# Optimization experiments

Hardware: AMD Instinct MI355X
Metric: run time of the kernel (lower is better)

Reference implementation:

```python
import jax, jax.numpy as jnp
import numpy as np

D_MODEL = 2048
N_HEADS = 32
N_KV_HEADS = 8
D_K = D_MODEL // N_HEADS
HEADS_PER_GROUP = N_HEADS // N_KV_HEADS
B, S = 2, 2048


def setup_inputs() -> dict:
    key = jax.random.key(0)
    ks = jax.random.split(key, 12)
    scale = 1.0 / np.sqrt(D_MODEL)
    inp = {
        "q": jax.random.normal(ks[0], (B, S, D_MODEL), jnp.float32),
        "k": jax.random.normal(ks[1], (B, S, D_MODEL), jnp.float32),
        "v": jax.random.normal(ks[2], (B, S, D_MODEL), jnp.float32),
        # causal mask, broadcastable over [B, H, S, S]
        "mask": jnp.tril(jnp.ones((S, S), jnp.bool_))[None, None],
        # torch Linear convention: W [out, in], y = x @ W.T + b
        "Wq": jax.random.normal(ks[3], (D_MODEL, D_MODEL), jnp.float32) * scale,
        "bq": jax.random.normal(ks[4], (D_MODEL,), jnp.float32) * 0.01,
        "Wk": jax.random.normal(ks[5], (N_KV_HEADS * D_K, D_MODEL), jnp.float32) * scale,
        "bk": jax.random.normal(ks[6], (N_KV_HEADS * D_K,), jnp.float32) * 0.01,
        "Wv": jax.random.normal(ks[7], (N_KV_HEADS * D_K, D_MODEL), jnp.float32) * scale,
        "bv": jax.random.normal(ks[8], (N_KV_HEADS * D_K,), jnp.float32) * 0.01,
        "Wo": jax.random.normal(ks[9], (D_MODEL, D_MODEL), jnp.float32) * scale,
        "bo": jax.random.normal(ks[10], (D_MODEL,), jnp.float32) * 0.01,
    }
    return inp


def reference(q, k, v, mask, Wq, bq, Wk, bk, Wv, bv, Wo, bo):
    b, s, _ = q.shape
    # projections (torch Linear: x @ W.T + b)
    query = q @ Wq.T + bq                      # [B, S, D]
    key = k @ Wk.T + bk                        # [B, S, Kv*dk]
    value = v @ Wv.T + bv
    # [B, Kv, G, S, dk] for query (group heads per kv head instead of repeating K/V)
    query = query.reshape(b, s, N_KV_HEADS, HEADS_PER_GROUP, D_K).transpose(0, 2, 3, 1, 4)
    key = key.reshape(b, s, N_KV_HEADS, D_K).transpose(0, 2, 1, 3)      # [B, Kv, S, dk]
    value = value.reshape(b, s, N_KV_HEADS, D_K).transpose(0, 2, 1, 3)  # [B, Kv, S, dk]
    scores = jnp.einsum('bkgqd,bksd->bkgqs', query, key) / jnp.sqrt(jnp.float32(D_K))
    # mask is [1,1,S,S] broadcastable; add group axis
    scores = jnp.where(mask[:, :, None], scores, jnp.float32(-1e9))
    attn = jax.nn.softmax(scores, axis=-1)     # dropout p=0.0 -> identity
    out = jnp.einsum('bkgqs,bksd->bkgqd', attn, value)  # [B, Kv, G, S, dk]
    out = out.transpose(0, 3, 1, 2, 4).reshape(b, s, D_MODEL)
    return out @ Wo.T + bo
```

## Files before the change

### kernel.cpp

```cpp
#include <hip/hip_runtime.h>
#include <cstdint>

#define D_MODEL 2048
#define NKV 8
#define GQ 4
#define DK 64
#define B_ 2
#define S_ 2048
#define MS (B_*S_)
#define KVD (NKV*DK)

typedef unsigned short u16;
typedef __attribute__((ext_vector_type(8))) short bf16x8;
typedef __attribute__((ext_vector_type(4))) short bf16x4;
typedef __attribute__((ext_vector_type(4))) float f32x4;
typedef __attribute__((ext_vector_type(16))) float f32x16;
typedef __attribute__((ext_vector_type(4))) unsigned short u16x4;

__device__ __forceinline__ u16 f2bf(float f) {
    union { float f; uint32_t u; } x; x.f = f;
    uint32_t u = x.u;
    uint32_t r = (u + 0x7FFFu + ((u >> 16) & 1u)) >> 16;
    return (u16)r;
}
__device__ __forceinline__ float bf2f(u16 h) {
    union { uint32_t u; float f; } x; x.u = ((uint32_t)h) << 16;
    return x.f;
}

__device__ __forceinline__ void gload_lds16(const void* g, void* lds) {
    __builtin_amdgcn_global_load_lds(
        (const __attribute__((address_space(1))) void*)g,
        (__attribute__((address_space(3))) void*)lds, 16, 0, 0);
}

__device__ __forceinline__ bf16x8 cvt8(float4 a, float4 b) {
    union { unsigned u[4]; bf16x8 v; } r;
    asm("v_cvt_pk_bf16_f32 %0, %1, %2" : "=v"(r.u[0]) : "v"(a.x), "v"(a.y));
    asm("v_cvt_pk_bf16_f32 %0, %1, %2" : "=v"(r.u[1]) : "v"(a.z), "v"(a.w));
    asm("v_cvt_pk_bf16_f32 %0, %1, %2" : "=v"(r.u[2]) : "v"(b.x), "v"(b.y));
    asm("v_cvt_pk_bf16_f32 %0, %1, %2" : "=v"(r.u[3]) : "v"(b.z), "v"(b.w));
    return r.v;
}

__global__ __launch_bounds__(256, 2)
void gemm_qkv(const float* __restrict__ Aq, const float* __restrict__ Ak,
              const float* __restrict__ Av,
              const float* __restrict__ Wq, const float* __restrict__ Wk,
              const float* __restrict__ Wv,
              const float* __restrict__ bq, const float* __restrict__ bk,
              const float* __restrict__ bv,
              u16* __restrict__ Qp, u16* __restrict__ Kp, u16* __restrict__ Vt) {
    __shared__ __align__(16) u16 SA[2][128 * 64];
    __shared__ __align__(16) u16 SB[2][128 * 64];
    const int tid = threadIdx.x;
    const int lane = tid & 63;
    const int fr = lane & 15, fq = lane >> 4;
    const int w = tid >> 6;
    const int wr = w >> 1, wc = w & 1;
    const int K = D_MODEL, NT = K / 64;

    const int bid = blockIdx.x;
    const int sw = (bid & 7) * 96 + (bid >> 3);
    const float* A; const float* Bw; const float* bias;
    int seg, by, bx;
    if (sw < 512)      { seg = 0; A = Aq; Bw = Wq; bias = bq; by = sw >> 4;         bx = sw & 15; }
    else if (sw < 640) { seg = 1; A = Ak; Bw = Wk; bias = bk; by = (sw - 512) >> 2; bx = (sw - 512) & 3; }
    else               { seg = 2; A = Av; Bw = Wv; bias = bv; by = (sw - 640) >> 2; bx = (sw - 640) & 3; }
    const int m0 = by * 128, n0 = bx * 128;

    const int sr = tid >> 3, sc = tid & 7;
    float4 ra[4][2], rb[4][2];
    auto LOADA = [&](int t) {
        const float* p0 = A + (size_t)(m0 + sr) * K + (t << 6) + sc * 8;
#pragma unroll
        for (int j = 0; j < 4; ++j) {
            const float* p = p0 + (size_t)(j * 32) * K;
            ra[j][0] = *(const float4*)p; ra[j][1] = *(const float4*)(p + 4);
        }
    };
    auto LOADB = [&](int t) {
        const float* p0 = Bw + (size_t)(n0 + sr) * K + (t << 6) + sc * 8;
#pragma unroll
        for (int j = 0; j < 4; ++j) {
            const float* p = p0 + (size_t)(j * 32) * K;
            rb[j][0] = *(const float4*)p; rb[j][1] = *(const float4*)(p + 4);
        }
    };
    auto WRITE = [&](int q) {
#pragma unroll
        for (int j = 0; j < 4; ++j) {
            int row = j * 32 + sr;
            *(bf16x8*)((char*)&SA[q][0] + row * 128 + ((sc ^ (row & 7)) * 16)) = cvt8(ra[j][0], ra[j][1]);
        }
#pragma unroll
        for (int j = 0; j < 4; ++j) {
            int row = j * 32 + sr;
            *(bf16x8*)((char*)&SB[q][0] + row * 128 + ((sc ^ (row & 7)) * 16)) = cvt8(rb[j][0], rb[j][1]);
        }
    };

    f32x4 acc[4][4] = {};
    const int arow = wr * 64, brow = wc * 64;

    LOADA(0); LOADB(0);
    WRITE(0);
    LOADA(1); LOADB(1);
    asm volatile("s_waitcnt lgkmcnt(0)" ::: "memory");
    __builtin_amdgcn_s_barrier();
    __builtin_amdgcn_sched_barrier(0);

    for (int t = 0; t < NT; ++t) {
        const int q = t & 1;
        if (t + 1 < NT) WRITE(q ^ 1);
        const char* sa = (const char*)&SA[q][0];
        const char* sb = (const char*)&SB[q][0];
#pragma unroll
        for (int kk = 0; kk < 2; ++kk) {
            const int cs = (((kk << 2) | fq) ^ (fr & 7)) * 16;
            bf16x8 af[4], bfr[4];
#pragma unroll
            for (int m = 0; m < 4; ++m)
                af[m] = *(const bf16x8*)(sa + (size_t)(arow + m * 16 + fr) * 128 + cs);
#pragma unroll
            for (int n = 0; n < 4; ++n)
                bfr[n] = *(const bf16x8*)(sb + (size_t)(brow + n * 16 + fr) * 128 + cs);
            __builtin_amdgcn_s_setprio(1);
#pragma unroll
            for (int m = 0; m < 4; ++m)
#pragma unroll
                for (int n = 0; n < 4; ++n)
                    acc[m][n] = __builtin_amdgcn_mfma_f32_16x16x32_bf16(af[m], bfr[n], acc[m][n], 0, 0, 0);
            __builtin_amdgcn_s_setprio(0);
        }
        if (t + 2 < NT) { LOADA(t + 2); LOADB(t + 2); }
        if (t + 1 < NT) {
            asm volatile("s_waitcnt lgkmcnt(0)" ::: "memory");
            __builtin_amdgcn_s_barrier();
            __builtin_amdgcn_sched_barrier(0);
        }
    }

    float bvv[4];
#pragma unroll
    for (int n = 0; n < 4; ++n) bvv[n] = bias[n0 + brow + n * 16 + fr];
#pragma unroll
    for (int m = 0; m < 4; ++m) {
        int grow0 = m0 + arow + m * 16 + fq * 4;
#pragma unroll
        for (int n = 0; n < 4; ++n) {
            int gcol = n0 + brow + n * 16 + fr;
#pragma unroll
            for (int r = 0; r < 4; ++r) {
                float v = acc[m][n][r] + bvv[n];
                int grow = grow0 + r;
                if (seg == 0)      Qp[(size_t)grow * D_MODEL + gcol] = f2bf(v);
                else if (seg == 1) Kp[(size_t)grow * KVD + gcol] = f2bf(v);
                else {
                    int b = grow >> 11, s = grow & (S_ - 1);
                    Vt[((size_t)b * KVD + gcol) * S_ + s] = f2bf(v);
                }
            }
        }
    }
}

__global__ __launch_bounds__(512, 2)
void gemm_o(const u16* __restrict__ A, const float* __restrict__ Bw,
            const float* __restrict__ bias, float* __restrict__ Cout) {
    __shared__ __align__(16) u16 SA[2][256 * 64];
    __shared__ __align__(16) u16 SB[2][128 * 64];
    const int tid = threadIdx.x;
    const int lane = tid & 63;
    const int fr = lane & 15, fq = lane >> 4;
    const int wid = tid >> 6;
    const int wr = wid >> 1, wc = wid & 1;
    const int K = D_MODEL, N = D_MODEL, NT = K / 64;

    const int bid = blockIdx.x;
    const int sw = (bid & 7) * 32 + (bid >> 3);
    const int by = sw >> 4, bx = sw & 15;
    const int m0 = by * 256, n0 = bx * 128;

    auto GLOADA = [&](int t, int q) {
        const int k0 = t << 6;
#pragma unroll
        for (int j = 0; j < 4; ++j) {
            int idx = tid + j * 512, row = idx >> 3, c = idx & 7;
            gload_lds16(A + (size_t)(m0 + row) * K + k0 + ((c ^ (row & 7)) * 8),
                        &SA[q][(j * 512 + (tid >> 6) * 64) * 8]);
        }
    };
    float4 rb[2][2];
    auto LOADB = [&](int t) {
        const int k0 = t << 6;
#pragma unroll
        for (int j = 0; j < 2; ++j) {
            int idx = tid + j * 512, row = idx >> 3, c = idx & 7;
            const float* p = Bw + (size_t)(n0 + row) * K + k0 + c * 8;
            rb[j][0] = *(const float4*)p;
            rb[j][1] = *(const float4*)(p + 4);
        }
    };
    auto WRITEB = [&](int q) {
#pragma unroll
        for (int j = 0; j < 2; ++j) {
            int idx = tid + j * 512, row = idx >> 3, c = idx & 7;
            *(bf16x8*)((char*)&SB[q][0] + row * 128 + ((c ^ (row & 7)) * 16)) = cvt8(rb[j][0], rb[j][1]);
        }
    };

    f32x4 acc[4][4] = {};
    const int arow = wr * 64, brow = wc * 64;

    GLOADA(0, 0);
    asm volatile("" ::: "memory");
    LOADB(0);
    WRITEB(0);
    GLOADA(1, 1);
    asm volatile("" ::: "memory");
    LOADB(1);
    asm volatile("s_waitcnt lgkmcnt(0)" ::: "memory");
    __builtin_amdgcn_s_barrier();

    for (int t = 0; t < NT; ++t) {
        const int q = t & 1;
        const char* sa = (const char*)&SA[q][0];
        const char* sb = (const char*)&SB[q][0];
#pragma unroll
        for (int kk = 0; kk < 2; ++kk) {
            const int cs = (((kk << 2) | fq) ^ (fr & 7)) * 16;
            bf16x8 af[4], bfr[4];
#pragma unroll
            for (int m = 0; m < 4; ++m)
                af[m] = *(const bf16x8*)(sa + (size_t)(arow + m * 16 + fr) * 128 + cs);
#pragma unroll
            for (int n = 0; n < 4; ++n)
                bfr[n] = *(const bf16x8*)(sb + (size_t)(brow + n * 16 + fr) * 128 + cs);
            __builtin_amdgcn_s_setprio(1);
#pragma unroll
            for (int m = 0; m < 4; ++m)
#pragma unroll
                for (int n = 0; n < 4; ++n)
                    acc[m][n] = __builtin_amdgcn_mfma_f32_16x16x32_bf16(af[m], bfr[n], acc[m][n], 0, 0, 0);
            __builtin_amdgcn_s_setprio(0);
        }
        asm volatile("s_barrier" ::: "memory");
        if (t + 1 < NT) {
            asm volatile("s_waitcnt vmcnt(4)" ::: "memory");
            WRITEB(q ^ 1);
            if (t + 2 < NT) {
                GLOADA(t + 2, q);
                asm volatile("" ::: "memory");
                LOADB(t + 2);
            }
            asm volatile("s_waitcnt lgkmcnt(0)" ::: "memory");
            __builtin_amdgcn_s_barrier();
        }
    }

    float bvv[4];
#pragma unroll
    for (int n = 0; n < 4; ++n) bvv[n] = bias[n0 + brow + n * 16 + fr];
#pragma unroll
    for (int m = 0; m < 4; ++m) {
        int grow0 = m0 + wr * 64 + m * 16 + fq * 4;
#pragma unroll
        for (int n = 0; n < 4; ++n) {
            int gcol = n0 + brow + n * 16 + fr;
#pragma unroll
            for (int r = 0; r < 4; ++r)
                Cout[(size_t)(grow0 + r) * N + gcol] = acc[m][n][r] + bvv[n];
        }
    }
}

__global__ __launch_bounds__(256, 4)
void attn_fwd(const u16* __restrict__ Qp, const u16* __restrict__ Kp,
              const u16* __restrict__ Vt, u16* __restrict__ AO) {
    __shared__ __align__(16) u16 Klds[2][4096];
    __shared__ __align__(16) u16 Vlds[2][4096];
    const int bid = blockIdx.x;
    const int qblk = 15 - (bid >> 6);
    const int rest = bid & 63;
    const int b = rest >> 5;
    const int kv = (rest >> 2) & 7;
    const int g = rest & 3;
    const int tid = threadIdx.x, w = tid >> 6, l = tid & 63;
    const int q31 = l & 31, hi = l >> 5;
    const int h = kv * GQ + g;
    const int qw = qblk * 128 + w * 32;
    const int q0 = qw + q31;

    const u16* kbase = Kp + (size_t)(b * S_) * KVD + kv * DK;
    const u16* vbase = Vt + ((size_t)b * KVD + kv * DK) * S_;

    const float SCALE = 0.125f * 1.44269504f;
    bf16x8 qf[4];
    const u16* qp = Qp + ((size_t)(b * S_) + q0) * D_MODEL + h * DK;
#pragma unroll
    for (int ks = 0; ks < 4; ++ks) {
        bf16x8 t = *(const bf16x8*)(qp + ks * 16 + hi * 8);
#pragma unroll
        for (int j = 0; j < 8; ++j) t[j] = (short)f2bf(bf2f((u16)t[j]) * SCALE);
        qf[ks] = t;
    }

    const int nt = 2 * qblk + 2;
    const int bound = (qw + 31) >> 6;

    auto STAGE = [&](int t, int bufsel) {
#pragma unroll
        for (int r = 0; r < 2; ++r) {
            int idx = r * 256 + tid;
            int row = idx >> 3;
            int slotK = (idx & 7) ^ (row & 7);
            int jV = (idx & 7) ^ ((row >> 1) & 7);
            u16* kdst = &Klds[bufsel][(r * 256 + w * 64) * 8];
            u16* vdst = &Vlds[bufsel][(r * 256 + w * 64) * 8];
            gload_lds16(kbase + (size_t)(t * 64 + row) * KVD + slotK * 8, kdst);
            gload_lds16(vbase + (size_t)row * S_ + t * 64 + jV * 8, vdst);
        }
    };

    f32x16 o0 = {}, o1 = {};
    float m_run = -1e30f, l_run = 0.f;

    STAGE(0, 0);
    __syncthreads();
    int cur = 0;
    for (int t = 0; t < nt; ++t) {
        if (t + 1 < nt) STAGE(t + 1, cur ^ 1);
        if (t <= bound) {
            const u16* Kc = Klds[cur];
            const u16* Vc = Vlds[cur];
            const int base0 = t * 64, base1 = t * 64 + 32;
            const bool act1 = (base1 <= qw + 31);

            f32x16 s0 = {};
            {
                const int row = q31;
#pragma unroll
                for (int ks = 0; ks < 4; ++ks) {
                    bf16x8 kf = *(const bf16x8*)&Kc[row * 64 + ((((ks << 1) | hi)) ^ (row & 7)) * 8];
                    s0 = __builtin_amdgcn_mfma_f32_32x32x16_bf16(kf, qf[ks], s0, 0, 0, 0);
                }
            }
            f32x16 s1 = {};
            if (act1) {
                const int row = 32 + q31;
#pragma unroll
                for (int ks = 0; ks < 4; ++ks) {
                    bf16x8 kf = *(const bf16x8*)&Kc[row * 64 + ((((ks << 1) | hi)) ^ (row & 7)) * 8];
                    s1 = __builtin_amdgcn_mfma_f32_32x32x16_bf16(kf, qf[ks], s1, 0, 0, 0);
                }
            }
            if (base0 + 31 > qw) {
#pragma unroll
                for (int r = 0; r < 16; ++r) {
                    int koff = (r & 3) + 8 * (r >> 2) + 4 * hi;
                    s0[r] = (base0 + koff <= q0) ? s0[r] : -1e30f;
                }
            }
            if (act1 && (base1 + 31 > qw)) {
#pragma unroll
                for (int r = 0; r < 16; ++r) {
                    int koff = (r & 3) + 8 * (r >> 2) + 4 * hi;
                    s1[r] = (base1 + koff <= q0) ? s1[r] : -1e30f;
                }
            }
            float pm = s0[0];
#pragma unroll
            for (int r = 1; r < 16; ++r) pm = fmaxf(pm, s0[r]);
            if (act1) {
#pragma unroll
                for (int r = 0; r < 16; ++r) pm = fmaxf(pm, s1[r]);
            }
            pm = fmaxf(pm, __shfl_xor(pm, 32));
            if (__any(pm > m_run + 8.0f)) {
                float mn = fmaxf(m_run, pm);
                float sc = __builtin_amdgcn_exp2f(m_run - mn);
                m_run = mn; l_run *= sc;
#pragma unroll
                for (int r = 0; r < 16; ++r) { o0[r] *= sc; o1[r] *= sc; }
            }
            float psum = 0.f;
#pragma unroll
            for (int r = 0; r < 16; ++r) { float p = __builtin_amdgcn_exp2f(s0[r] - m_run); s0[r] = p; psum += p; }
            if (act1) {
#pragma unroll
                for (int r = 0; r < 16; ++r) { float p = __builtin_amdgcn_exp2f(s1[r] - m_run); s1[r] = p; psum += p; }
            }
            l_run += psum;
            unsigned W0[8], W1[8];
#pragma unroll
            for (int tt = 0; tt < 8; ++tt)
                asm("v_cvt_pk_bf16_f32 %0, %1, %2" : "=v"(W0[tt]) : "v"(s0[2 * tt]), "v"(s0[2 * tt + 1]));
            if (act1) {
#pragma unroll
                for (int tt = 0; tt < 8; ++tt)
                    asm("v_cvt_pk_bf16_f32 %0, %1, %2" : "=v"(W1[tt]) : "v"(s1[2 * tt]), "v"(s1[2 * tt + 1]));
            }
#pragma unroll
            for (int sl = 0; sl < 2; ++sl) {
                union { unsigned u[4]; bf16x8 v; } bw;
#pragma unroll
                for (int i = 0; i < 4; ++i) bw.u[i] = W0[sl * 4 + i];
#pragma unroll
                for (int half = 0; half < 2; ++half) {
                    const int row = half * 32 + q31;
                    union { bf16x4 h4[2]; bf16x8 v; } vf;
                    int sa = (sl * 4 + hi) ^ (row & 14);
                    int sb = (sl * 4 + 2 + hi) ^ (row & 14);
                    vf.h4[0] = *(const bf16x4*)&Vc[row * 64 + sa * 4];
                    vf.h4[1] = *(const bf16x4*)&Vc[row * 64 + sb * 4];
                    if (half == 0) o0 = __builtin_amdgcn_mfma_f32_32x32x16_bf16(vf.v, bw.v, o0, 0, 0, 0);
                    else           o1 = __builtin_amdgcn_mfma_f32_32x32x16_bf16(vf.v, bw.v, o1, 0, 0, 0);
                }
            }
            if (act1) {
#pragma unroll
                for (int sl = 2; sl < 4; ++sl) {
                    union { unsigned u[4]; bf16x8 v; } bw;
#pragma unroll
                    for (int i = 0; i < 4; ++i) bw.u[i] = W1[(sl - 2) * 4 + i];
#pragma unroll
                    for (int half = 0; half < 2; ++half) {
                        const int row = half * 32 + q31;
                        union { bf16x4 h4[2]; bf16x8 v; } vf;
                        int sa = (sl * 4 + hi) ^ (row & 14);
                        int sb = (sl * 4 + 2 + hi) ^ (row & 14);
                        vf.h4[0] = *(const bf16x4*)&Vc[row * 64 + sa * 4];
                        vf.h4[1] = *(const bf16x4*)&Vc[row * 64 + sb * 4];
                        if (half == 0) o0 = __builtin_amdgcn_mfma_f32_32x32x16_bf16(vf.v, bw.v, o0, 0, 0, 0);
                        else           o1 = __builtin_amdgcn_mfma_f32_32x32x16_bf16(vf.v, bw.v, o1, 0, 0, 0);
                    }
                }
            }
        }
        __syncthreads();
        cur ^= 1;
    }

    float lt = l_run + __shfl_xor(l_run, 32);
    float rl = 1.0f / lt;
    u16* op = AO + ((size_t)(b * S_) + q0) * D_MODEL + h * DK;
#pragma unroll
    for (int half = 0; half < 2; ++half) {
#pragma unroll
        for (int rr = 0; rr < 16; rr += 4) {
            u16x4 pk;
#pragma unroll
            for (int i = 0; i < 4; ++i)
                pk[i] = f2bf((half ? o1[rr + i] : o0[rr + i]) * rl);
            *(u16x4*)(op + half * 32 + (rr >> 2) * 8 + 4 * hi) = pk;
        }
    }
}

extern "C" void kernel_launch(void* const* d_in, const int* in_sizes, int n_in,
                              void* d_out, int out_size, void* d_ws, size_t ws_size,
                              hipStream_t stream) {
    const float* q  = (const float*)d_in[0];
    const float* k  = (const float*)d_in[1];
    const float* v  = (const float*)d_in[2];
    const float* Wq = (const float*)d_in[4];
    const float* bq = (const float*)d_in[5];
    const float* Wk = (const float*)d_in[6];
    const float* bk = (const float*)d_in[7];
    const float* Wv = (const float*)d_in[8];
    const float* bv = (const float*)d_in[9];
    const float* Wo = (const float*)d_in[10];
    const float* bo = (const float*)d_in[11];
    float* out = (float*)d_out;

    char* ws = (char*)d_ws;
    size_t off = 0;
    auto alloc = [&](size_t bytes) -> void* {
        void* p = ws + off;
        off += (bytes + 255) & ~(size_t)255;
        return p;
    };
    u16* Qp = (u16*)alloc((size_t)MS * D_MODEL * 2);
    u16* Kp = (u16*)alloc((size_t)MS * KVD * 2);
    u16* Vt = (u16*)alloc((size_t)MS * KVD * 2);
    u16* AO = (u16*)alloc((size_t)MS * D_MODEL * 2);

    gemm_qkv<<<768, 256, 0, stream>>>(q, k, v, Wq, Wk, Wv, bq, bk, bv, Qp, Kp, Vt);

    attn_fwd<<<16 * 64, 256, 0, stream>>>(Qp, Kp, Vt, AO);

    gemm_o<<<256, 512, 0, stream>>>(AO, Wo, bo, out);
}
```

Before: 209.5 us.

## Halve GEMM K-tile to 32 and shrink output projection tile to 128x128

Both projection GEMMs now stage K-slices of 32 instead of 64, which halves shared memory per block and raises the occupancy hint to 3 blocks per CU. The output GEMM drops its 256x128 tile, 512-thread blocks and async global-to-LDS loads for A, and instead uses the same register-staged 128x128 tile with 256 threads and 512 blocks. The global loads for the next tile are issued before the MFMA work rather than after it. In exchange there are twice as many barriers per K sweep and less data reuse per tile in the output GEMM.

```diff
diff --git a/kernel.cpp b/kernel.cpp
--- a/kernel.cpp
+++ b/kernel.cpp
@@ -43,7 +43,7 @@
     return r.v;
 }
 
-__global__ __launch_bounds__(256, 2)
+__global__ __launch_bounds__(256, 3)
 void gemm_qkv(const float* __restrict__ Aq, const float* __restrict__ Ak,
               const float* __restrict__ Av,
               const float* __restrict__ Wq, const float* __restrict__ Wk,
@@ -51,14 +51,14 @@
               const float* __restrict__ bq, const float* __restrict__ bk,
               const float* __restrict__ bv,
               u16* __restrict__ Qp, u16* __restrict__ Kp, u16* __restrict__ Vt) {
-    __shared__ __align__(16) u16 SA[2][128 * 64];
-    __shared__ __align__(16) u16 SB[2][128 * 64];
+    __shared__ __align__(16) u16 SA[2][128 * 32];
+    __shared__ __align__(16) u16 SB[2][128 * 32];
     const int tid = threadIdx.x;
     const int lane = tid & 63;
     const int fr = lane & 15, fq = lane >> 4;
     const int w = tid >> 6;
     const int wr = w >> 1, wc = w & 1;
-    const int K = D_MODEL, NT = K / 64;
+    const int K = D_MODEL, NT = K / 32;
 
     const int bid = blockIdx.x;
     const int sw = (bid & 7) * 96 + (bid >> 3);
@@ -69,34 +69,31 @@
     else               { seg = 2; A = Av; Bw = Wv; bias = bv; by = (sw - 640) >> 2; bx = (sw - 640) & 3; }
     const int m0 = by * 128, n0 = bx * 128;
 
-    const int sr = tid >> 3, sc = tid & 7;
-    float4 ra[4][2], rb[4][2];
+    const int sr = tid >> 2, sc = tid & 3;
+    float4 ra[2][2], rb[2][2];
     auto LOADA = [&](int t) {
-        const float* p0 = A + (size_t)(m0 + sr) * K + (t << 6) + sc * 8;
-#pragma unroll
-        for (int j = 0; j < 4; ++j) {
-            const float* p = p0 + (size_t)(j * 32) * K;
+        const float* p0 = A + (size_t)(m0 + sr) * K + (t << 5) + sc * 8;
+#pragma unroll
+        for (int j = 0; j < 2; ++j) {
+            const float* p = p0 + (size_t)(j * 64) * K;
             ra[j][0] = *(const float4*)p; ra[j][1] = *(const float4*)(p + 4);
         }
     };
     auto LOADB = [&](int t) {
-        const float* p0 = Bw + (size_t)(n0 + sr) * K + (t << 6) + sc * 8;
-#pragma unroll
-        for (int j = 0; j < 4; ++j) {
-            const float* p = p0 + (size_t)(j * 32) * K;
+        const float* p0 = Bw + (size_t)(n0 + sr) * K + (t << 5) + sc * 8;
+#pragma unroll
+        for (int j = 0; j < 2; ++j) {
+            const float* p = p0 + (size_t)(j * 64) * K;
             rb[j][0] = *(const float4*)p; rb[j][1] = *(const float4*)(p + 4);
         }
     };
     auto WRITE = [&](int q) {
 #pragma unroll
-        for (int j = 0; j < 4; ++j) {
-            int row = j * 32 + sr;
-            *(bf16x8*)((char*)&SA[q][0] + row * 128 + ((sc ^ (row & 7)) * 16)) = cvt8(ra[j][0], ra[j][1]);
-        }
-#pragma unroll
-        for (int j = 0; j < 4; ++j) {
-            int row = j * 32 + sr;
-            *(bf16x8*)((char*)&SB[q][0] + row * 128 + ((sc ^ (row & 7)) * 16)) = cvt8(rb[j][0], rb[j][1]);
+        for (int j = 0; j < 2; ++j) {
+            int row = j * 64 + sr;
+            int s = (sc ^ ((row >> 1) & 3)) << 4;
+            *(bf16x8*)((char*)&SA[q][0] + row * 64 + s) = cvt8(ra[j][0], ra[j][1]);
+            *(bf16x8*)((char*)&SB[q][0] + row * 64 + s) = cvt8(rb[j][0], rb[j][1]);
         }
     };
 
@@ -108,37 +105,33 @@
     LOADA(1); LOADB(1);
     asm volatile("s_waitcnt lgkmcnt(0)" ::: "memory");
     __builtin_amdgcn_s_barrier();
-    __builtin_amdgcn_sched_barrier(0);
 
     for (int t = 0; t < NT; ++t) {
         const int q = t & 1;
         if (t + 1 < NT) WRITE(q ^ 1);
+        if (t + 2 < NT) { LOADA(t + 2); LOADB(t + 2); }
         const char* sa = (const char*)&SA[q][0];
         const char* sb = (const char*)&SB[q][0];
-#pragma unroll
-        for (int kk = 0; kk < 2; ++kk) {
-            const int cs = (((kk << 2) | fq) ^ (fr & 7)) * 16;
-            bf16x8 af[4], bfr[4];
-#pragma unroll
-            for (int m = 0; m < 4; ++m)
-                af[m] = *(const bf16x8*)(sa + (size_t)(arow + m * 16 + fr) * 128 + cs);
+        bf16x8 af[4], bfr[4];
+#pragma unroll
+        for (int m = 0; m < 4; ++m) {
+            int row = arow + m * 16 + fr;
+            af[m] = *(const bf16x8*)(sa + row * 64 + ((fq ^ ((row >> 1) & 3)) << 4));
+        }
+#pragma unroll
+        for (int n = 0; n < 4; ++n) {
+            int row = brow + n * 16 + fr;
+            bfr[n] = *(const bf16x8*)(sb + row * 64 + ((fq ^ ((row >> 1) & 3)) << 4));
+        }
+        __builtin_amdgcn_s_setprio(1);
+#pragma unroll
+        for (int m = 0; m < 4; ++m)
 #pragma unroll
             for (int n = 0; n < 4; ++n)
-                bfr[n] = *(const bf16x8*)(sb + (size_t)(brow + n * 16 + fr) * 128 + cs);
-            __builtin_amdgcn_s_setprio(1);
-#pragma unroll
-            for (int m = 0; m < 4; ++m)
-#pragma unroll
-                for (int n = 0; n < 4; ++n)
-                    acc[m][n] = __builtin_amdgcn_mfma_f32_16x16x32_bf16(af[m], bfr[n], acc[m][n], 0, 0, 0);
-            __builtin_amdgcn_s_setprio(0);
-        }
-        if (t + 2 < NT) { LOADA(t + 2); LOADB(t + 2); }
-        if (t + 1 < NT) {
-            asm volatile("s_waitcnt lgkmcnt(0)" ::: "memory");
-            __builtin_amdgcn_s_barrier();
-            __builtin_amdgcn_sched_barrier(0);
-        }
+                acc[m][n] = __builtin_amdgcn_mfma_f32_16x16x32_bf16(af[m], bfr[n], acc[m][n], 0, 0, 0);
+        __builtin_amdgcn_s_setprio(0);
+        asm volatile("s_waitcnt lgkmcnt(0)" ::: "memory");
+        __builtin_amdgcn_s_barrier();
     }
 
     float bvv[4];
@@ -165,98 +158,85 @@
     }
 }
 
-__global__ __launch_bounds__(512, 2)
+__global__ __launch_bounds__(256, 3)
 void gemm_o(const u16* __restrict__ A, const float* __restrict__ Bw,
             const float* __restrict__ bias, float* __restrict__ Cout) {
-    __shared__ __align__(16) u16 SA[2][256 * 64];
-    __shared__ __align__(16) u16 SB[2][128 * 64];
+    __shared__ __align__(16) u16 SA[2][128 * 32];
+    __shared__ __align__(16) u16 SB[2][128 * 32];
     const int tid = threadIdx.x;
     const int lane = tid & 63;
     const int fr = lane & 15, fq = lane >> 4;
-    const int wid = tid >> 6;
-    const int wr = wid >> 1, wc = wid & 1;
-    const int K = D_MODEL, N = D_MODEL, NT = K / 64;
+    const int w = tid >> 6;
+    const int wr = w >> 1, wc = w & 1;
+    const int K = D_MODEL, N = D_MODEL, NT = K / 32;
 
     const int bid = blockIdx.x;
-    const int sw = (bid & 7) * 32 + (bid >> 3);
+    const int sw = (bid & 7) * 64 + (bid >> 3);
     const int by = sw >> 4, bx = sw & 15;
-    const int m0 = by * 256, n0 = bx * 128;
-
-    auto GLOADA = [&](int t, int q) {
-        const int k0 = t << 6;
-#pragma unroll
-        for (int j = 0; j < 4; ++j) {
-            int idx = tid + j * 512, row = idx >> 3, c = idx & 7;
-            gload_lds16(A + (size_t)(m0 + row) * K + k0 + ((c ^ (row & 7)) * 8),
-                        &SA[q][(j * 512 + (tid >> 6) * 64) * 8]);
-        }
-    };
+    const int m0 = by * 128, n0 = bx * 128;
+
+    const int sr = tid >> 2, sc = tid & 3;
+    bf16x8 rA[2];
     float4 rb[2][2];
+    auto LOADA = [&](int t) {
+        const u16* p0 = A + (size_t)(m0 + sr) * K + (t << 5) + sc * 8;
+#pragma unroll
+        for (int j = 0; j < 2; ++j)
+            rA[j] = *(const bf16x8*)(p0 + (size_t)(j * 64) * K);
+    };
     auto LOADB = [&](int t) {
-        const int k0 = t << 6;
+        const float* p0 = Bw + (size_t)(n0 + sr) * K + (t << 5) + sc * 8;
 #pragma unroll
         for (int j = 0; j < 2; ++j) {
-            int idx = tid + j * 512, row = idx >> 3, c = idx & 7;
-            const float* p = Bw + (size_t)(n0 + row) * K + k0 + c * 8;
-            rb[j][0] = *(const float4*)p;
-            rb[j][1] = *(const float4*)(p + 4);
-        }
-    };
-    auto WRITEB = [&](int q) {
+            const float* p = p0 + (size_t)(j * 64) * K;
+            rb[j][0] = *(const float4*)p; rb[j][1] = *(const float4*)(p + 4);
+        }
+    };
+    auto WRITE = [&](int q) {
 #pragma unroll
         for (int j = 0; j < 2; ++j) {
-            int idx = tid + j * 512, row = idx >> 3, c = idx & 7;
-            *(bf16x8*)((char*)&SB[q][0] + row * 128 + ((c ^ (row & 7)) * 16)) = cvt8(rb[j][0], rb[j][1]);
+            int row = j * 64 + sr;
+            int s = (sc ^ ((row >> 1) & 3)) << 4;
+            *(bf16x8*)((char*)&SA[q][0] + row * 64 + s) = rA[j];
+            *(bf16x8*)((char*)&SB[q][0] + row * 64 + s) = cvt8(rb[j][0], rb[j][1]);
         }
     };
 
     f32x4 acc[4][4] = {};
     const int arow = wr * 64, brow = wc * 64;
 
-    GLOADA(0, 0);
-    asm volatile("" ::: "memory");
-    LOADB(0);
-    WRITEB(0);
-    GLOADA(1, 1);
-    asm volatile("" ::: "memory");
-    LOADB(1);
+    LOADA(0); LOADB(0);
+    WRITE(0);
+    LOADA(1); LOADB(1);
     asm volatile("s_waitcnt lgkmcnt(0)" ::: "memory");
     __builtin_amdgcn_s_barrier();
 
     for (int t = 0; t < NT; ++t) {
         const int q = t & 1;
+        if (t + 1 < NT) WRITE(q ^ 1);
+        if (t + 2 < NT) { LOADA(t + 2); LOADB(t + 2); }
         const char* sa = (const char*)&SA[q][0];
         const char* sb = (const char*)&SB[q][0];
-#pragma unroll
-        for (int kk = 0; kk < 2; ++kk) {
-            const int cs = (((kk << 2) | fq) ^ (fr & 7)) * 16;
-            bf16x8 af[4], bfr[4];
-#pragma unroll
-            for (int m = 0; m < 4; ++m)
-                af[m] = *(const bf16x8*)(sa + (size_t)(arow + m * 16 + fr) * 128 + cs);
+        bf16x8 af[4], bfr[4];
+#pragma unroll
+        for (int m = 0; m < 4; ++m) {
+            int row = arow + m * 16 + fr;
+            af[m] = *(const bf16x8*)(sa + row * 64 + ((fq ^ ((row >> 1) & 3)) << 4));
+        }
+#pragma unroll
+        for (int n = 0; n < 4; ++n) {
+            int row = brow + n * 16 + fr;
+            bfr[n] = *(const bf16x8*)(sb + row * 64 + ((fq ^ ((row >> 1) & 3)) << 4));
+        }
+        __builtin_amdgcn_s_setprio(1);
+#pragma unroll
+        for (int m = 0; m < 4; ++m)
 #pragma unroll
             for (int n = 0; n < 4; ++n)
-                bfr[n] = *(const bf16x8*)(sb + (size_t)(brow + n * 16 + fr) * 128 + cs);
-            __builtin_amdgcn_s_setprio(1);
-#pragma unroll
-            for (int m = 0; m < 4; ++m)
-#pragma unroll
-                for (int n = 0; n < 4; ++n)
-                    acc[m][n] = __builtin_amdgcn_mfma_f32_16x16x32_bf16(af[m], bfr[n], acc[m][n], 0, 0, 0);
-            __builtin_amdgcn_s_setprio(0);
-        }
-        asm volatile("s_barrier" ::: "memory");
-        if (t + 1 < NT) {
-            asm volatile("s_waitcnt vmcnt(4)" ::: "memory");
-            WRITEB(q ^ 1);
-            if (t + 2 < NT) {
-                GLOADA(t + 2, q);
-                asm volatile("" ::: "memory");
-                LOADB(t + 2);
-            }
-            asm volatile("s_waitcnt lgkmcnt(0)" ::: "memory");
-            __builtin_amdgcn_s_barrier();
-        }
+                acc[m][n] = __builtin_amdgcn_mfma_f32_16x16x32_bf16(af[m], bfr[n], acc[m][n], 0, 0, 0);
+        __builtin_amdgcn_s_setprio(0);
+        asm volatile("s_waitcnt lgkmcnt(0)" ::: "memory");
+        __builtin_amdgcn_s_barrier();
     }
 
     float bvv[4];
@@ -264,7 +244,7 @@
     for (int n = 0; n < 4; ++n) bvv[n] = bias[n0 + brow + n * 16 + fr];
 #pragma unroll
     for (int m = 0; m < 4; ++m) {
-        int grow0 = m0 + wr * 64 + m * 16 + fq * 4;
+        int grow0 = m0 + arow + m * 16 + fq * 4;
 #pragma unroll
         for (int n = 0; n < 4; ++n) {
             int gcol = n0 + brow + n * 16 + fr;
@@ -490,5 +470,5 @@
 
     attn_fwd<<<16 * 64, 256, 0, stream>>>(Qp, Kp, Vt, AO);
 
-    gemm_o<<<256, 512, 0, stream>>>(AO, Wo, bo, out);
-}
+    gemm_o<<<512, 256, 0, stream>>>(AO, Wo, bo, out);
+}
```

Result: faster. 197.7 us (-5.6%).
